# Kernel optimization log

Hardware: AMD Instinct MI355X
Metric: run time of the kernel (lower is better)

The kernel has to match this reference:

```python
import jax, jax.numpy as jnp
import numpy as np

N_OSC = 256
BATCH = 1024
DT = 0.1
STEPS = 10


def setup_inputs() -> dict:
    key = jax.random.key(0)
    k_theta, k_K, k_omega = jax.random.split(key, 3)
    theta_init = jax.random.normal(k_theta, (BATCH, N_OSC), dtype=jnp.float32)
    K0 = jax.random.normal(k_K, (N_OSC, N_OSC), dtype=jnp.float32) * 0.1
    K = (K0 + K0.T) / 2  # symmetric coupling matrix, as in torch init
    omega = jax.random.normal(k_omega, (N_OSC,), dtype=jnp.float32) * 0.1
    K_global = jnp.float32(0.5)
    return {"theta_init": theta_init, "K": K, "omega": omega, "K_global": K_global}


def reference(theta_init, K, omega, K_global):
    n = K.shape[0]

    def step(theta, _):
        # diff[b, i, j] = theta[b, j] - theta[b, i]
        diff = theta[..., None, :] - theta[..., :, None]
        coupling_sum = jnp.sum(K * jnp.sin(diff), axis=-1)  # (batch, n)
        dtheta = omega + (K_global / n) * coupling_sum
        theta_new = theta + DT * dtheta
        # wrap to (-pi, pi]
        theta_new = jnp.arctan2(jnp.sin(theta_new), jnp.cos(theta_new))
        return theta_new, None

    theta, _ = jax.lax.scan(step, theta_init, None, length=STEPS)
    cos_mean = jnp.cos(theta).mean(axis=-1)
    sin_mean = jnp.sin(theta).mean(axis=-1)
    coherence = jnp.sqrt(cos_mean ** 2 + sin_mean ** 2)
    return theta, coherence
```

## Files before the change

### kernel.cpp

```cpp
#include <hip/hip_runtime.h>
#include <math.h>


typedef __attribute__((ext_vector_type(4))) float f32x4;
typedef __attribute__((ext_vector_type(2))) long long2_t;

constexpr int N       = 256;
constexpr int RB      = 16;
constexpr int STEPS   = 10;
constexpr int WAVES   = 8;
constexpr int THREADS = WAVES * 64;
constexpr float DT    = 0.1f;
constexpr float TWO_PI     = 6.28318530717958648f;
constexpr float INV_TWO_PI = 0.15915494309189535f;

__global__ __launch_bounds__(THREADS, 2)
void kuramoto_r10(const float* __restrict__ theta0,
                  const float* __restrict__ Kmat,
                  const float* __restrict__ omega,
                  const float* __restrict__ kglob,
                  float* __restrict__ theta_out,
                  float* __restrict__ coh_out)
{
    __shared__ __align__(16) unsigned char KF[N * N];
    __shared__ __align__(16) unsigned char SC[2][RB * 512];
    __shared__ float redS[RB][WAVES], redC[RB][WAVES];

    const int tid  = threadIdx.x;
    const int wv   = tid >> 6;
    const int lane = tid & 63;
    const int q    = lane >> 4;
    const int l15  = lane & 15;
    const int b0   = blockIdx.x * RB;

    const float kgn = kglob[0] * (1.0f / 256.0f);

    float th[8], om[8], sn[8], cs[8];
#pragma unroll
    for (int t = 0; t < 2; ++t) {
        const int ob = 32 * wv + 16 * t + 4 * q;
        float4 t4 = *(const float4*)(theta0 + (size_t)(b0 + l15) * N + ob);
        float4 o4 = *(const float4*)(omega + ob);
        th[4*t+0] = t4.x; th[4*t+1] = t4.y; th[4*t+2] = t4.z; th[4*t+3] = t4.w;
        om[4*t+0] = o4.x; om[4*t+1] = o4.y; om[4*t+2] = o4.z; om[4*t+3] = o4.w;
    }

#pragma unroll 4
    for (int i = 0; i < 16; ++i) {
        const int g   = i * THREADS + tid;
        const int row = g >> 5;
        const int u8  = g & 31;
        const float* src = Kmat + (size_t)g * 8;
        float4 lo = *(const float4*)src;
        float4 hi = *(const float4*)(src + 4);
        int w0 = __builtin_amdgcn_cvt_pk_fp8_f32(lo.x, lo.y, 0, false);
        w0     = __builtin_amdgcn_cvt_pk_fp8_f32(lo.z, lo.w, w0, true);
        int w1 = __builtin_amdgcn_cvt_pk_fp8_f32(hi.x, hi.y, 0, false);
        w1     = __builtin_amdgcn_cvt_pk_fp8_f32(hi.z, hi.w, w1, true);
        const int id = ((row >> 4) << 9) | ((u8 >> 2) << 6) | ((u8 & 3) << 4) | (row & 15);
        int2 outp; outp.x = w0; outp.y = w1;
        *(int2*)(KF + (size_t)id * 8) = outp;
    }

#pragma unroll
    for (int k = 0; k < 8; ++k)
        __sincosf(th[k], &sn[k], &cs[k]);

    __syncthreads();

    long kf[2][8];
#pragma unroll
    for (int t = 0; t < 2; ++t) {
        const unsigned char* base = KF + (size_t)((2 * wv + t) * 512 + lane) * 8;
#pragma unroll
        for (int c = 0; c < 8; ++c)
            kf[t][c] = *(const long*)(base + (size_t)c * 512);
    }

    const int so = 4 * (q & 1);
    const int g0 = 4 * wv + (q >> 1);

    for (int s = 0; s < STEPS; ++s) {
        unsigned char* rowp = &SC[s & 1][l15 * 512];
#pragma unroll
        for (int t = 0; t < 2; ++t) {
            int spk = __builtin_amdgcn_cvt_pk_fp8_f32(sn[4*t+0], sn[4*t+1], 0, false);
            spk     = __builtin_amdgcn_cvt_pk_fp8_f32(sn[4*t+2], sn[4*t+3], spk, true);
            int cpk = __builtin_amdgcn_cvt_pk_fp8_f32(cs[4*t+0], cs[4*t+1], 0, false);
            cpk     = __builtin_amdgcn_cvt_pk_fp8_f32(cs[4*t+2], cs[4*t+3], cpk, true);
            const int base = (((g0 + 2 * t) ^ l15) << 4);
            *(int*)(rowp + base + so)     = spk;
            *(int*)(rowp + base + 8 + so) = cpk;
        }
        __syncthreads();

        f32x4 aS[2], aC[2];
        aS[0] = (f32x4){0.f,0.f,0.f,0.f}; aS[1] = (f32x4){0.f,0.f,0.f,0.f};
        aC[0] = (f32x4){0.f,0.f,0.f,0.f}; aC[1] = (f32x4){0.f,0.f,0.f,0.f};
#pragma unroll
        for (int c = 0; c < 8; ++c) {
            long2_t v = *(const long2_t*)(rowp + ((((4 * c + q) ^ l15)) << 4));
            aS[0] = __builtin_amdgcn_mfma_f32_16x16x32_fp8_fp8(kf[0][c], v.x, aS[0], 0, 0, 0);
            aC[0] = __builtin_amdgcn_mfma_f32_16x16x32_fp8_fp8(kf[0][c], v.y, aC[0], 0, 0, 0);
            aS[1] = __builtin_amdgcn_mfma_f32_16x16x32_fp8_fp8(kf[1][c], v.x, aS[1], 0, 0, 0);
            aC[1] = __builtin_amdgcn_mfma_f32_16x16x32_fp8_fp8(kf[1][c], v.y, aC[1], 0, 0, 0);
        }

#pragma unroll
        for (int t = 0; t < 2; ++t)
#pragma unroll
            for (int r = 0; r < 4; ++r) {
                const int k = 4 * t + r;
                float coup = cs[k] * aS[t][r] - sn[k] * aC[t][r];
                float d  = DT * fmaf(kgn, coup, om[k]);
                float d2 = d * d;
                float sd = d * fmaf(d2, -1.0f / 6.0f, 1.0f);
                float cd = fmaf(d2, fmaf(d2, 1.0f / 24.0f, -0.5f), 1.0f);
                float s2 = fmaf(sn[k], cd,  cs[k] * sd);
                float c2 = fmaf(cs[k], cd, -sn[k] * sd);
                sn[k] = s2; cs[k] = c2; th[k] += d;
            }
    }

    float ps = 0.f, pc = 0.f;
#pragma unroll
    for (int t = 0; t < 2; ++t) {
        const int ob = 32 * wv + 16 * t + 4 * q;
        float4 outv;
        outv.x = fmaf(-TWO_PI, rintf(th[4*t+0] * INV_TWO_PI), th[4*t+0]);
        outv.y = fmaf(-TWO_PI, rintf(th[4*t+1] * INV_TWO_PI), th[4*t+1]);
        outv.z = fmaf(-TWO_PI, rintf(th[4*t+2] * INV_TWO_PI), th[4*t+2]);
        outv.w = fmaf(-TWO_PI, rintf(th[4*t+3] * INV_TWO_PI), th[4*t+3]);
        *(float4*)(theta_out + (size_t)(b0 + l15) * N + ob) = outv;
#pragma unroll
        for (int r = 0; r < 4; ++r) { ps += sn[4*t+r]; pc += cs[4*t+r]; }
    }
    ps += __shfl_xor(ps, 16, 64);  pc += __shfl_xor(pc, 16, 64);
    ps += __shfl_xor(ps, 32, 64);  pc += __shfl_xor(pc, 32, 64);
    if (q == 0) { redS[l15][wv] = ps; redC[l15][wv] = pc; }
    __syncthreads();
    if (tid < RB) {
        float S = 0.f, C = 0.f;
#pragma unroll
        for (int k = 0; k < WAVES; ++k) { S += redS[tid][k]; C += redC[tid][k]; }
        float sm = S * (1.0f / 256.0f);
        float cm = C * (1.0f / 256.0f);
        coh_out[b0 + tid] = sqrtf(sm * sm + cm * cm);
    }
}

extern "C" void kernel_launch(void* const* d_in, const int* in_sizes, int n_in,
                              void* d_out, int out_size, void* d_ws, size_t ws_size,
                              hipStream_t stream) {
    const float* theta0 = (const float*)d_in[0];
    const float* Kmat   = (const float*)d_in[1];
    const float* omega  = (const float*)d_in[2];
    const float* kglob  = (const float*)d_in[3];

    (void)d_ws; (void)ws_size;

    float* theta_out = (float*)d_out;
    float* coh_out   = theta_out + 1024 * N;

    kuramoto_r10<<<dim3(1024 / RB), dim3(THREADS), 0, stream>>>(
        theta0, Kmat, omega, kglob, theta_out, coh_out);
}
```

Baseline: 72.59 us.

## Double waves per block to one 16-row K tile each, swizzle K LDS

Raises the block to 16 waves so each wave owns one 16-oscillator output tile instead of two, halving per-wave MFMA chains, register state and K conversion work. The MFMA loop splits K into two independent accumulator chains that are summed afterwards. K is stored in LDS with an XOR swizzle to reduce bank conflicts on the fragment loads. The trade is more waves per block and costlier barriers, and the min-blocks occupancy hint is dropped.

After: 70.92 us. -2.3%, faster.

```diff
diff --git a/kernel.cpp b/kernel.cpp
--- a/kernel.cpp
+++ b/kernel.cpp
@@ -8,14 +8,14 @@
 constexpr int N       = 256;
 constexpr int RB      = 16;
 constexpr int STEPS   = 10;
-constexpr int WAVES   = 8;
+constexpr int WAVES   = 16;
 constexpr int THREADS = WAVES * 64;
 constexpr float DT    = 0.1f;
 constexpr float TWO_PI     = 6.28318530717958648f;
 constexpr float INV_TWO_PI = 0.15915494309189535f;
 
-__global__ __launch_bounds__(THREADS, 2)
-void kuramoto_r10(const float* __restrict__ theta0,
+__global__ __launch_bounds__(THREADS)
+void kuramoto_r11(const float* __restrict__ theta0,
                   const float* __restrict__ Kmat,
                   const float* __restrict__ omega,
                   const float* __restrict__ kglob,
@@ -35,18 +35,17 @@
 
     const float kgn = kglob[0] * (1.0f / 256.0f);
 
-    float th[8], om[8], sn[8], cs[8];
-#pragma unroll
-    for (int t = 0; t < 2; ++t) {
-        const int ob = 32 * wv + 16 * t + 4 * q;
+    float th[4], om[4], sn[4], cs[4];
+    {
+        const int ob = 16 * wv + 4 * q;
         float4 t4 = *(const float4*)(theta0 + (size_t)(b0 + l15) * N + ob);
         float4 o4 = *(const float4*)(omega + ob);
-        th[4*t+0] = t4.x; th[4*t+1] = t4.y; th[4*t+2] = t4.z; th[4*t+3] = t4.w;
-        om[4*t+0] = o4.x; om[4*t+1] = o4.y; om[4*t+2] = o4.z; om[4*t+3] = o4.w;
+        th[0]=t4.x; th[1]=t4.y; th[2]=t4.z; th[3]=t4.w;
+        om[0]=o4.x; om[1]=o4.y; om[2]=o4.z; om[3]=o4.w;
     }
 
 #pragma unroll 4
-    for (int i = 0; i < 16; ++i) {
+    for (int i = 0; i < 8; ++i) {
         const int g   = i * THREADS + tid;
         const int row = g >> 5;
         const int u8  = g & 31;
@@ -58,82 +57,79 @@
         int w1 = __builtin_amdgcn_cvt_pk_fp8_f32(hi.x, hi.y, 0, false);
         w1     = __builtin_amdgcn_cvt_pk_fp8_f32(hi.z, hi.w, w1, true);
         const int id = ((row >> 4) << 9) | ((u8 >> 2) << 6) | ((u8 & 3) << 4) | (row & 15);
+        const int ph = id ^ ((id >> 4) & 15);
         int2 outp; outp.x = w0; outp.y = w1;
-        *(int2*)(KF + (size_t)id * 8) = outp;
+        *(int2*)(KF + (size_t)ph * 8) = outp;
     }
 
 #pragma unroll
-    for (int k = 0; k < 8; ++k)
+    for (int k = 0; k < 4; ++k)
         __sincosf(th[k], &sn[k], &cs[k]);
 
     __syncthreads();
 
-    long kf[2][8];
+    long kf[8];
 #pragma unroll
-    for (int t = 0; t < 2; ++t) {
-        const unsigned char* base = KF + (size_t)((2 * wv + t) * 512 + lane) * 8;
-#pragma unroll
-        for (int c = 0; c < 8; ++c)
-            kf[t][c] = *(const long*)(base + (size_t)c * 512);
+    for (int c = 0; c < 8; ++c) {
+        const int id = (wv << 9) | (c << 6) | lane;
+        const int ph = id ^ ((id >> 4) & 15);
+        kf[c] = *(const long*)(KF + (size_t)ph * 8);
     }
 
     const int so = 4 * (q & 1);
-    const int g0 = 4 * wv + (q >> 1);
+    const int su = 2 * wv + (q >> 1);
 
     for (int s = 0; s < STEPS; ++s) {
         unsigned char* rowp = &SC[s & 1][l15 * 512];
-#pragma unroll
-        for (int t = 0; t < 2; ++t) {
-            int spk = __builtin_amdgcn_cvt_pk_fp8_f32(sn[4*t+0], sn[4*t+1], 0, false);
-            spk     = __builtin_amdgcn_cvt_pk_fp8_f32(sn[4*t+2], sn[4*t+3], spk, true);
-            int cpk = __builtin_amdgcn_cvt_pk_fp8_f32(cs[4*t+0], cs[4*t+1], 0, false);
-            cpk     = __builtin_amdgcn_cvt_pk_fp8_f32(cs[4*t+2], cs[4*t+3], cpk, true);
-            const int base = (((g0 + 2 * t) ^ l15) << 4);
+        {
+            int spk = __builtin_amdgcn_cvt_pk_fp8_f32(sn[0], sn[1], 0, false);
+            spk     = __builtin_amdgcn_cvt_pk_fp8_f32(sn[2], sn[3], spk, true);
+            int cpk = __builtin_amdgcn_cvt_pk_fp8_f32(cs[0], cs[1], 0, false);
+            cpk     = __builtin_amdgcn_cvt_pk_fp8_f32(cs[2], cs[3], cpk, true);
+            const int base = ((su ^ l15) << 4);
             *(int*)(rowp + base + so)     = spk;
             *(int*)(rowp + base + 8 + so) = cpk;
         }
         __syncthreads();
 
-        f32x4 aS[2], aC[2];
-        aS[0] = (f32x4){0.f,0.f,0.f,0.f}; aS[1] = (f32x4){0.f,0.f,0.f,0.f};
-        aC[0] = (f32x4){0.f,0.f,0.f,0.f}; aC[1] = (f32x4){0.f,0.f,0.f,0.f};
+        f32x4 aS0 = (f32x4){0.f,0.f,0.f,0.f}, aS1 = (f32x4){0.f,0.f,0.f,0.f};
+        f32x4 aC0 = (f32x4){0.f,0.f,0.f,0.f}, aC1 = (f32x4){0.f,0.f,0.f,0.f};
 #pragma unroll
-        for (int c = 0; c < 8; ++c) {
-            long2_t v = *(const long2_t*)(rowp + ((((4 * c + q) ^ l15)) << 4));
-            aS[0] = __builtin_amdgcn_mfma_f32_16x16x32_fp8_fp8(kf[0][c], v.x, aS[0], 0, 0, 0);
-            aC[0] = __builtin_amdgcn_mfma_f32_16x16x32_fp8_fp8(kf[0][c], v.y, aC[0], 0, 0, 0);
-            aS[1] = __builtin_amdgcn_mfma_f32_16x16x32_fp8_fp8(kf[1][c], v.x, aS[1], 0, 0, 0);
-            aC[1] = __builtin_amdgcn_mfma_f32_16x16x32_fp8_fp8(kf[1][c], v.y, aC[1], 0, 0, 0);
+        for (int c = 0; c < 4; ++c) {
+            long2_t v1 = *(const long2_t*)(rowp + (((4*c +      q) ^ l15) << 4));
+            long2_t v2 = *(const long2_t*)(rowp + (((4*c + 16 + q) ^ l15) << 4));
+            aS0 = __builtin_amdgcn_mfma_f32_16x16x32_fp8_fp8(kf[c],   v1.x, aS0, 0, 0, 0);
+            aC0 = __builtin_amdgcn_mfma_f32_16x16x32_fp8_fp8(kf[c],   v1.y, aC0, 0, 0, 0);
+            aS1 = __builtin_amdgcn_mfma_f32_16x16x32_fp8_fp8(kf[c+4], v2.x, aS1, 0, 0, 0);
+            aC1 = __builtin_amdgcn_mfma_f32_16x16x32_fp8_fp8(kf[c+4], v2.y, aC1, 0, 0, 0);
         }
+        f32x4 aS = aS0 + aS1;
+        f32x4 aC = aC0 + aC1;
 
 #pragma unroll
-        for (int t = 0; t < 2; ++t)
-#pragma unroll
-            for (int r = 0; r < 4; ++r) {
-                const int k = 4 * t + r;
-                float coup = cs[k] * aS[t][r] - sn[k] * aC[t][r];
-                float d  = DT * fmaf(kgn, coup, om[k]);
-                float d2 = d * d;
-                float sd = d * fmaf(d2, -1.0f / 6.0f, 1.0f);
-                float cd = fmaf(d2, fmaf(d2, 1.0f / 24.0f, -0.5f), 1.0f);
-                float s2 = fmaf(sn[k], cd,  cs[k] * sd);
-                float c2 = fmaf(cs[k], cd, -sn[k] * sd);
-                sn[k] = s2; cs[k] = c2; th[k] += d;
-            }
+        for (int r = 0; r < 4; ++r) {
+            float coup = cs[r] * aS[r] - sn[r] * aC[r];
+            float d  = DT * fmaf(kgn, coup, om[r]);
+            float d2 = d * d;
+            float sd = d * fmaf(d2, -1.0f / 6.0f, 1.0f);
+            float cd = fmaf(d2, fmaf(d2, 1.0f / 24.0f, -0.5f), 1.0f);
+            float s2 = fmaf(sn[r], cd,  cs[r] * sd);
+            float c2 = fmaf(cs[r], cd, -sn[r] * sd);
+            sn[r] = s2; cs[r] = c2; th[r] += d;
+        }
     }
 
     float ps = 0.f, pc = 0.f;
-#pragma unroll
-    for (int t = 0; t < 2; ++t) {
-        const int ob = 32 * wv + 16 * t + 4 * q;
+    {
+        const int ob = 16 * wv + 4 * q;
         float4 outv;
-        outv.x = fmaf(-TWO_PI, rintf(th[4*t+0] * INV_TWO_PI), th[4*t+0]);
-        outv.y = fmaf(-TWO_PI, rintf(th[4*t+1] * INV_TWO_PI), th[4*t+1]);
-        outv.z = fmaf(-TWO_PI, rintf(th[4*t+2] * INV_TWO_PI), th[4*t+2]);
-        outv.w = fmaf(-TWO_PI, rintf(th[4*t+3] * INV_TWO_PI), th[4*t+3]);
+        outv.x = fmaf(-TWO_PI, rintf(th[0] * INV_TWO_PI), th[0]);
+        outv.y = fmaf(-TWO_PI, rintf(th[1] * INV_TWO_PI), th[1]);
+        outv.z = fmaf(-TWO_PI, rintf(th[2] * INV_TWO_PI), th[2]);
+        outv.w = fmaf(-TWO_PI, rintf(th[3] * INV_TWO_PI), th[3]);
         *(float4*)(theta_out + (size_t)(b0 + l15) * N + ob) = outv;
 #pragma unroll
-        for (int r = 0; r < 4; ++r) { ps += sn[4*t+r]; pc += cs[4*t+r]; }
+        for (int r = 0; r < 4; ++r) { ps += sn[r]; pc += cs[r]; }
     }
     ps += __shfl_xor(ps, 16, 64);  pc += __shfl_xor(pc, 16, 64);
     ps += __shfl_xor(ps, 32, 64);  pc += __shfl_xor(pc, 32, 64);
@@ -162,6 +158,6 @@
     float* theta_out = (float*)d_out;
     float* coh_out   = theta_out + 1024 * N;
 
-    kuramoto_r10<<<dim3(1024 / RB), dim3(THREADS), 0, stream>>>(
+    kuramoto_r11<<<dim3(1024 / RB), dim3(THREADS), 0, stream>>>(
         theta0, Kmat, omega, kglob, theta_out, coh_out);
 }
```
